# Optimization experiments

Measured on AMD Instinct MI355X. Metric: run time of the kernel, lower is better.

Reference implementation:

```python
import jax, jax.numpy as jnp
import numpy as np
from jax import lax

DIM = 128
N_CODEBOOKS = 8
CODEBOOK_SIZE = 2048
BATCH = 16
TOKENS = 2048


def setup_inputs() -> dict:
    key = jax.random.key(0)
    k1, k2 = jax.random.split(key)
    x = jax.random.normal(k1, (BATCH, DIM, TOKENS), dtype=jnp.float32)
    # matches nn.Parameter(torch.randn(K, D) / D**0.5) per stage, stacked
    codebooks = jax.random.normal(k2, (N_CODEBOOKS, CODEBOOK_SIZE, DIM),
                                  dtype=jnp.float32) / jnp.sqrt(jnp.float32(DIM))
    return {"x": x, "codebooks": codebooks}


def reference(x, codebooks):
    """Residual VQ forward.

    x: (B, D, T), codebooks: (n_cb, K, D)
    Returns (total_quantized (B,D,T), codes (B,n_cb,T) int32, commitment_loss scalar)
    """
    xt = jnp.transpose(x, (0, 2, 1))  # (B, T, D)

    def step(carry, cb):
        residual, total = carry  # (B,T,D) each; cb: (K,D)
        # squared euclidean distances: ||r||^2 - 2 r.c + ||c||^2 -> (B,T,K)
        dist = (jnp.sum(residual * residual, axis=-1, keepdims=True)
                - 2.0 * jnp.einsum('btd,kd->btk', residual, cb)
                + jnp.sum(cb * cb, axis=-1))
        idx = jnp.argmin(dist, axis=-1)          # (B, T)
        quantized = cb[idx]                       # gather -> (B, T, D)
        # straight-through combine
        q_st = residual + lax.stop_gradient(quantized - residual)
        total = total + q_st
        residual = residual - lax.stop_gradient(quantized)
        # F.mse_loss(residual.detach(), zeros) == mean(residual**2), detached
        loss = jnp.mean(lax.stop_gradient(residual) ** 2)
        return (residual, total), (idx.astype(jnp.int32), loss)

    init = (xt, jnp.zeros_like(xt))
    (_, total), (codes, losses) = lax.scan(step, init, codebooks)
    total_quantized = jnp.transpose(total, (0, 2, 1))   # (B, D, T)
    codes = jnp.transpose(codes, (1, 0, 2))             # (B, n_cb, T)
    commitment_loss = jnp.sum(losses)
    return total_quantized, codes, commitment_loss
```

## Files before the change

kernel.cpp:

```cpp
#include <hip/hip_runtime.h>

#define DIM 128
#define NCB 8
#define KSZ 2048
#define BATCH 16
#define TOK 2048
#define NTOK (BATCH * TOK)
#define NELEM (BATCH * DIM * TOK)
#define T_TILE 64
#define NTHR 512
#define CHUNK 64
#define HCHUNKS 16

typedef float f32x4 __attribute__((ext_vector_type(4)));
typedef short s16x8 __attribute__((ext_vector_type(8)));

__device__ __forceinline__ unsigned short f2bf(float f) {
    unsigned u = __float_as_uint(f);
    u = (u + 0x7FFFu + ((u >> 16) & 1u)) >> 16;
    return (unsigned short)u;
}
__device__ __forceinline__ float bf2f(unsigned short h) {
    return __uint_as_float(((unsigned)h) << 16);
}

__global__ void rvq_prep_hi(const float* __restrict__ cbs,
                            unsigned short* __restrict__ ch) {
    int i = blockIdx.x * 256 + threadIdx.x;
    ch[i] = f2bf(cbs[i]);
}

__global__ void rvq_cnorm(const float* __restrict__ cbs,
                          float* __restrict__ cnorm,
                          float* __restrict__ loss_acc) {
    if (blockIdx.x == 0 && threadIdx.x == 0) *loss_acc = 0.0f;
    int k = blockIdx.x * 256 + threadIdx.x;
    const float4* row = (const float4*)(cbs + (size_t)k * DIM);
    float s = 0.0f;
#pragma unroll
    for (int i = 0; i < DIM / 4; ++i) {
        float4 v = row[i];
        s += v.x * v.x + v.y * v.y + v.z * v.z + v.w * v.w;
    }
    cnorm[k] = s;
}

__global__ __launch_bounds__(NTHR, 4) void rvq_fused(
        const float* __restrict__ x,
        const float* __restrict__ cbs,
        const unsigned short* __restrict__ ch,
        const float* __restrict__ cng,
        float* __restrict__ out,
        float* __restrict__ codes,
        float* __restrict__ loss_acc) {
    __shared__ float res_lds[T_TILE][DIM + 2];
    __shared__ __align__(16) unsigned char uni[32768];
    unsigned short* Bb = (unsigned short*)uni;
    float*          mv1 = (float*)uni;
    float*          mv2 = (float*)(uni + 8192);
    unsigned short* mi1 = (unsigned short*)(uni + 16384);
    unsigned short* mi2 = (unsigned short*)(uni + 20480);
    unsigned short (*best4s)[4] = (unsigned short(*)[4])(uni + 24576);

    const int tid   = threadIdx.x;
    const int lane  = tid & 63;
    const int wv    = __builtin_amdgcn_readfirstlane(tid >> 6);
    const int col16 = lane & 15;
    const int quad  = lane >> 4;
    const int h2    = wv & 1;
    const int wg    = wv >> 1;

    const int token0 = blockIdx.x * T_TILE;
    const int b      = token0 >> 11;
    const int t_in_b = token0 & (TOK - 1);

    {
        const float* xb = x + (size_t)b * DIM * TOK + t_in_b;
#pragma unroll
        for (int it = 0; it < 4; ++it) {
            int idx = it * NTHR + tid;
            int d  = idx >> 4;
            int t4 = (idx & 15) * 4;
            float4 v = *(const float4*)(xb + (size_t)d * TOK + t4);
            res_lds[t4 + 0][d] = v.x;
            res_lds[t4 + 1][d] = v.y;
            res_lds[t4 + 2][d] = v.z;
            res_lds[t4 + 3][d] = v.w;
        }
    }
    __syncthreads();

    float my_loss = 0.0f;

#define STAGE_LOAD(cc)                                                         \
    {                                                                          \
        const unsigned short* _p = ch_s +                                      \
            ((size_t)(h2 * 1024 + (cc) * CHUNK + wg * 16 + col16)) * DIM +     \
            quad * 8;                                                          \
        stg0 = *(const s16x8*)(_p + 0);                                        \
        stg1 = *(const s16x8*)(_p + 32);                                       \
        stg2 = *(const s16x8*)(_p + 64);                                       \
        stg3 = *(const s16x8*)(_p + 96);                                       \
    }

#define STAGE_WRITE()                                                          \
    {                                                                          \
        unsigned short* _bh = Bb + h2 * 8192;                                  \
        *(s16x8*)&_bh[(wg * 4 + 0) * 512 + lane * 8] = stg0;                   \
        *(s16x8*)&_bh[(wg * 4 + 1) * 512 + lane * 8] = stg1;                   \
        *(s16x8*)&_bh[(wg * 4 + 2) * 512 + lane * 8] = stg2;                   \
        *(s16x8*)&_bh[(wg * 4 + 3) * 512 + lane * 8] = stg3;                   \
    }

#define COMPUTE_FOLD(cc)                                                       \
    {                                                                          \
        const unsigned short* _bh = Bb + h2 * 8192;                            \
        f32x4 a0 = (f32x4){0.f, 0.f, 0.f, 0.f};                                \
        f32x4 a1 = a0, a2 = a0, a3 = a0;                                       \
        _Pragma("unroll")                                                      \
        for (int dc = 0; dc < 4; ++dc) {                                       \
            s16x8 b0 = *(const s16x8*)&_bh[(0  + dc) * 512 + lane * 8];        \
            s16x8 b1 = *(const s16x8*)&_bh[(4  + dc) * 512 + lane * 8];        \
            s16x8 b2 = *(const s16x8*)&_bh[(8  + dc) * 512 + lane * 8];        \
            s16x8 b3 = *(const s16x8*)&_bh[(12 + dc) * 512 + lane * 8];        \
            a0 = __builtin_amdgcn_mfma_f32_16x16x32_bf16(ah[dc], b0, a0, 0, 0, 0); \
            a1 = __builtin_amdgcn_mfma_f32_16x16x32_bf16(ah[dc], b1, a1, 0, 0, 0); \
            a2 = __builtin_amdgcn_mfma_f32_16x16x32_bf16(ah[dc], b2, a2, 0, 0, 0); \
            a3 = __builtin_amdgcn_mfma_f32_16x16x32_bf16(ah[dc], b3, a3, 0, 0, 0); \
            a0 = __builtin_amdgcn_mfma_f32_16x16x32_bf16(al[dc], b0, a0, 0, 0, 0); \
            a1 = __builtin_amdgcn_mfma_f32_16x16x32_bf16(al[dc], b1, a1, 0, 0, 0); \
            a2 = __builtin_amdgcn_mfma_f32_16x16x32_bf16(al[dc], b2, a2, 0, 0, 0); \
            a3 = __builtin_amdgcn_mfma_f32_16x16x32_bf16(al[dc], b3, a3, 0, 0, 0); \
        }                                                                      \
        const int _ib0 = h2 * 1024 + (cc) * CHUNK + col16;                     \
        const float _cn0 = cn_s[_ib0], _cn1 = cn_s[_ib0 + 16];                 \
        const float _cn2 = cn_s[_ib0 + 32], _cn3 = cn_s[_ib0 + 48];            \
        _Pragma("unroll")                                                      \
        for (int r = 0; r < 4; ++r) {                                          \
            float p0 = fmaf(-2.0f, a0[r], _cn0);                               \
            float p1 = fmaf(-2.0f, a1[r], _cn1);                               \
            float p2 = fmaf(-2.0f, a2[r], _cn2);                               \
            float p3 = fmaf(-2.0f, a3[r], _cn3);                               \
            bool c01 = p1 < p0;                                                \
            float m01 = c01 ? p1 : p0; int j01 = c01 ? _ib0 + 16 : _ib0;       \
            bool c23 = p3 < p2;                                                \
            float m23 = c23 ? p3 : p2; int j23 = c23 ? _ib0 + 48 : _ib0 + 32;  \
            bool cf = m23 < m01;                                               \
            float m = cf ? m23 : m01; int jm = cf ? j23 : j01;                 \
            bool b1 = m < v1[r];                                               \
            bool b2 = m < v2[r];                                               \
            v2[r] = b1 ? v1[r] : (b2 ? m : v2[r]);                             \
            i2[r] = b1 ? i1[r] : (b2 ? jm : i2[r]);                            \
            v1[r] = b1 ? m : v1[r];                                            \
            i1[r] = b1 ? jm : i1[r];                                           \
        }                                                                      \
    }

#pragma unroll 1
    for (int s = 0; s < NCB; ++s) {
        const unsigned short* __restrict__ ch_s = ch  + (size_t)s * KSZ * DIM;
        const float* __restrict__ cb_s = cbs + (size_t)s * KSZ * DIM;
        const float* __restrict__ cn_s = cng + (size_t)s * KSZ;

        s16x8 stg0, stg1, stg2, stg3;

        STAGE_LOAD(0);

        s16x8 ah[4], al[4];
#pragma unroll
        for (int dc = 0; dc < 4; ++dc) {
            int t  = wg * 16 + col16;
            int d0 = dc * 32 + quad * 8;
            float4 u = *(const float4*)&res_lds[t][d0];
            float4 w = *(const float4*)&res_lds[t][d0 + 4];
            float e[8] = {u.x, u.y, u.z, u.w, w.x, w.y, w.z, w.w};
            s16x8 hv, lv;
#pragma unroll
            for (int j = 0; j < 8; ++j) {
                unsigned short hb = f2bf(e[j]);
                hv[j] = (short)hb;
                lv[j] = (short)f2bf(e[j] - bf2f(hb));
            }
            ah[dc] = hv; al[dc] = lv;
        }

        float v1[4], v2[4]; int i1[4], i2[4];
#pragma unroll
        for (int r = 0; r < 4; ++r) {
            v1[r] = 3.4e38f; v2[r] = 3.4e38f; i1[r] = 0; i2[r] = 0;
        }

        STAGE_WRITE(); __syncthreads();
#pragma unroll 1
        for (int cc = 0; cc < HCHUNKS - 1; ++cc) {
            STAGE_LOAD(cc + 1);
            COMPUTE_FOLD(cc);
            __syncthreads();
            STAGE_WRITE();
            __syncthreads();
        }
        COMPUTE_FOLD(HCHUNKS - 1);
        __syncthreads();

#pragma unroll
        for (int r = 0; r < 4; ++r) {
            int t = wg * 16 + quad * 4 + r;
            int o = t * 32 + h2 * 16 + col16;
            mv1[o] = v1[r];
            mi1[o] = (unsigned short)i1[r];
            mv2[o] = v2[r];
            mi2[o] = (unsigned short)i2[r];
        }
        __syncthreads();

        {
            const int mt = tid >> 3;
            const int c8 = tid & 7;
            float bv[4] = {3.4e38f, 3.4e38f, 3.4e38f, 3.4e38f};
            int   bi[4] = {0x7FFFFFFF, 0x7FFFFFFF, 0x7FFFFFFF, 0x7FFFFFFF};
            const float* MV = (c8 & 4) ? mv2 : mv1;
            const unsigned short* MI = (c8 & 4) ? mi2 : mi1;
            const int base = mt * 32 + (c8 & 3) * 8;
            const float4 va = *(const float4*)&MV[base];
            const float4 vb = *(const float4*)&MV[base + 4];
            const s16x8  qi = *(const s16x8*)&MI[base];
            float vv[8] = {va.x, va.y, va.z, va.w, vb.x, vb.y, vb.z, vb.w};
#pragma unroll
            for (int c = 0; c < 8; ++c) {
                float v = vv[c]; int i = (int)(unsigned short)qi[c];
#pragma unroll
                for (int j = 0; j < 4; ++j) {
                    if (v < bv[j] || (v == bv[j] && i < bi[j])) {
                        float tv = bv[j]; bv[j] = v; v = tv;
                        int   ti = bi[j]; bi[j] = i; i = ti;
                    }
                }
            }
#pragma unroll
            for (int mk = 1; mk <= 4; mk <<= 1) {
                float ov[4]; int oi[4];
#pragma unroll
                for (int j = 0; j < 4; ++j) {
                    ov[j] = __shfl_xor(bv[j], mk, 64);
                    oi[j] = __shfl_xor(bi[j], mk, 64);
                }
#pragma unroll
                for (int c = 0; c < 4; ++c) {
                    float v = ov[c]; int i = oi[c];
#pragma unroll
                    for (int j = 0; j < 4; ++j) {
                        if (v < bv[j] || (v == bv[j] && i < bi[j])) {
                            float tv = bv[j]; bv[j] = v; v = tv;
                            int   ti = bi[j]; bi[j] = i; i = ti;
                        }
                    }
                }
            }
            if (c8 < 4) best4s[mt][c8] = (unsigned short)bi[c8];
        }
        __syncthreads();

        {
            const int t  = tid >> 3;
            const int c8 = tid & 7;
            const int cand = best4s[t][c8 & 3];
            const float* crow = cb_s + (size_t)cand * DIM;
            float n0 = 0, n1 = 0, n2 = 0, n3 = 0;
            float a0 = 0, a1 = 0, a2 = 0, a3 = 0;
#pragma unroll 8
            for (int d4 = 0; d4 < DIM / 4; ++d4) {
                float4 r4 = *(const float4*)&res_lds[t][d4 * 4];
                float4 q4 = *(const float4*)&crow[d4 * 4];
                n0 = fmaf(r4.x, r4.x, n0); n1 = fmaf(r4.y, r4.y, n1);
                n2 = fmaf(r4.z, r4.z, n2); n3 = fmaf(r4.w, r4.w, n3);
                a0 = fmaf(r4.x, q4.x, a0); a1 = fmaf(r4.y, q4.y, a1);
                a2 = fmaf(r4.z, q4.z, a2); a3 = fmaf(r4.w, q4.w, a3);
            }
            float rn  = (n0 + n1) + (n2 + n3);
            float dot = (a0 + a1) + (a2 + a3);
            float dist = fmaf(-2.0f, dot, rn) + cn_s[cand];
            int best = cand;
#pragma unroll
            for (int mk = 1; mk <= 2; mk <<= 1) {
                float od = __shfl_xor(dist, mk, 64);
                int   oi = __shfl_xor(best, mk, 64);
                if (od < dist || (od == dist && oi < best)) {
                    dist = od; best = oi;
                }
            }
            if (c8 == 0)
                codes[(size_t)b * (NCB * TOK) + (size_t)s * TOK + t_in_b + t] =
                    (float)best;
            const float* qrow = cb_s + (size_t)best * DIM;
            float lp = 0.0f;
#pragma unroll
            for (int k4 = 0; k4 < 4; ++k4) {
                int d = c8 * 16 + k4 * 4;
                float4 r4 = *(const float4*)&res_lds[t][d];
                float4 q4 = *(const float4*)&qrow[d];
                float4 nr;
                nr.x = r4.x - q4.x; nr.y = r4.y - q4.y;
                nr.z = r4.z - q4.z; nr.w = r4.w - q4.w;
                *(float4*)&res_lds[t][d] = nr;
                lp += nr.x * nr.x + nr.y * nr.y + nr.z * nr.z + nr.w * nr.w;
            }
            my_loss += lp;
        }
        __syncthreads();
    }

    {
        const float* xb = x + (size_t)b * DIM * TOK + t_in_b;
        float* ob = out + (size_t)b * DIM * TOK + t_in_b;
#pragma unroll
        for (int it = 0; it < 4; ++it) {
            int idx = it * NTHR + tid;
            int d  = idx >> 4;
            int t4 = (idx & 15) * 4;
            float4 v = *(const float4*)(xb + (size_t)d * TOK + t4);
            float4 o;
            o.x = v.x - res_lds[t4 + 0][d];
            o.y = v.y - res_lds[t4 + 1][d];
            o.z = v.z - res_lds[t4 + 2][d];
            o.w = v.w - res_lds[t4 + 3][d];
            *(float4*)(ob + (size_t)d * TOK + t4) = o;
        }
    }

#pragma unroll
    for (int off = 32; off > 0; off >>= 1)
        my_loss += __shfl_down(my_loss, off, 64);
    if (lane == 0) atomicAdd(loss_acc, my_loss);
}

__global__ void rvq_loss_fin(const float* __restrict__ loss_acc,
                             float* __restrict__ loss_out) {
    *loss_out = *loss_acc * (1.0f / (float)NELEM);
}

extern "C" void kernel_launch(void* const* d_in, const int* in_sizes, int n_in,
                              void* d_out, int out_size, void* d_ws, size_t ws_size,
                              hipStream_t stream) {
    const float* x   = (const float*)d_in[0];
    const float* cbs = (const float*)d_in[1];

    float* out      = (float*)d_out;
    float* codes    = out + NELEM;
    float* loss_out = out + NELEM + (size_t)BATCH * NCB * TOK;

    float* wsf      = (float*)d_ws;
    float* loss_acc = wsf;
    unsigned short* ch = (unsigned short*)(wsf + 256);
    float* cng = (float*)(ch + (size_t)NCB * KSZ * DIM);

    hipLaunchKernelGGL(rvq_prep_hi, dim3((NCB * KSZ * DIM) / 256), dim3(256),
                       0, stream, cbs, ch);
    hipLaunchKernelGGL(rvq_cnorm, dim3((NCB * KSZ) / 256), dim3(256), 0, stream,
                       cbs, cng, loss_acc);
    hipLaunchKernelGGL(rvq_fused, dim3(NTOK / T_TILE), dim3(NTHR), 0, stream,
                       x, cbs, ch, cng, out, codes, loss_acc);
    hipLaunchKernelGGL(rvq_loss_fin, dim3(1), dim3(1), 0, stream,
                       loss_acc, loss_out);
}
```

Baseline: 574.4 us.

## Shrink token tile, keep residuals in registers, double-buffer codebook via LDS DMA

Each block now handles 32 tokens with 2 waves instead of 64 tokens with 8 waves. Each wave scans the full codebook for its 16 tokens, where before the codebook was split into halves across wave pairs. Residuals stay in registers across stages instead of shared memory, and codebook chunks are double-buffered into LDS with global_load_lds, which drops the register staging and one barrier per chunk. MFMA sections get raised wave priority. The cost is twice as many blocks, each reading the whole codebook per stage, so total codebook traffic per token tile doubles, and occupancy now depends on register pressure from the rr array.

```diff
diff --git a/kernel.cpp b/kernel.cpp
--- a/kernel.cpp
+++ b/kernel.cpp
@@ -7,10 +7,10 @@
 #define TOK 2048
 #define NTOK (BATCH * TOK)
 #define NELEM (BATCH * DIM * TOK)
-#define T_TILE 64
-#define NTHR 512
+#define T_TILE 32
+#define NTHR 128
 #define CHUNK 64
-#define HCHUNKS 16
+#define NCHUNK (KSZ / CHUNK)
 
 typedef float f32x4 __attribute__((ext_vector_type(4)));
 typedef short s16x8 __attribute__((ext_vector_type(8)));
@@ -22,6 +22,12 @@
 }
 __device__ __forceinline__ float bf2f(unsigned short h) {
     return __uint_as_float(((unsigned)h) << 16);
+}
+
+__device__ __forceinline__ void gll16(const void* g, void* l) {
+    __builtin_amdgcn_global_load_lds(
+        (const __attribute__((address_space(1))) unsigned int*)g,
+        (__attribute__((address_space(3))) unsigned int*)l, 16, 0, 0);
 }
 
 __global__ void rvq_prep_hi(const float* __restrict__ cbs,
@@ -45,7 +51,7 @@
     cnorm[k] = s;
 }
 
-__global__ __launch_bounds__(NTHR, 4) void rvq_fused(
+__global__ __launch_bounds__(NTHR, 2) void rvq_fused(
         const float* __restrict__ x,
         const float* __restrict__ cbs,
         const unsigned short* __restrict__ ch,
@@ -53,22 +59,22 @@
         float* __restrict__ out,
         float* __restrict__ codes,
         float* __restrict__ loss_acc) {
-    __shared__ float res_lds[T_TILE][DIM + 2];
-    __shared__ __align__(16) unsigned char uni[32768];
-    unsigned short* Bb = (unsigned short*)uni;
+    __shared__ __attribute__((aligned(16))) unsigned char uni[32768];
+    __shared__ unsigned short best4s[T_TILE][4];
+
+    unsigned short* Bb  = (unsigned short*)uni;
+    float*          xs  = (float*)uni;
     float*          mv1 = (float*)uni;
-    float*          mv2 = (float*)(uni + 8192);
-    unsigned short* mi1 = (unsigned short*)(uni + 16384);
-    unsigned short* mi2 = (unsigned short*)(uni + 20480);
-    unsigned short (*best4s)[4] = (unsigned short(*)[4])(uni + 24576);
+    float*          mv2 = (float*)(uni + 2048);
+    unsigned short* mi1 = (unsigned short*)(uni + 4096);
+    unsigned short* mi2 = (unsigned short*)(uni + 5120);
 
     const int tid   = threadIdx.x;
     const int lane  = tid & 63;
     const int wv    = __builtin_amdgcn_readfirstlane(tid >> 6);
     const int col16 = lane & 15;
     const int quad  = lane >> 4;
-    const int h2    = wv & 1;
-    const int wg    = wv >> 1;
+    const int t_loc = wv * 16 + col16;
 
     const int token0 = blockIdx.x * T_TILE;
     const int b      = token0 >> 11;
@@ -77,46 +83,49 @@
     {
         const float* xb = x + (size_t)b * DIM * TOK + t_in_b;
 #pragma unroll
-        for (int it = 0; it < 4; ++it) {
+        for (int it = 0; it < 8; ++it) {
             int idx = it * NTHR + tid;
-            int d  = idx >> 4;
-            int t4 = (idx & 15) * 4;
+            int d  = idx >> 3;
+            int t4 = (idx & 7) * 4;
             float4 v = *(const float4*)(xb + (size_t)d * TOK + t4);
-            res_lds[t4 + 0][d] = v.x;
-            res_lds[t4 + 1][d] = v.y;
-            res_lds[t4 + 2][d] = v.z;
-            res_lds[t4 + 3][d] = v.w;
+            xs[(t4 + 0) * DIM + d] = v.x;
+            xs[(t4 + 1) * DIM + d] = v.y;
+            xs[(t4 + 2) * DIM + d] = v.z;
+            xs[(t4 + 3) * DIM + d] = v.w;
         }
     }
     __syncthreads();
 
+    float rr[4][8];
+#pragma unroll
+    for (int dc = 0; dc < 4; ++dc) {
+        float4 u = *(const float4*)&xs[t_loc * DIM + dc * 32 + quad * 8];
+        float4 w = *(const float4*)&xs[t_loc * DIM + dc * 32 + quad * 8 + 4];
+        rr[dc][0] = u.x; rr[dc][1] = u.y; rr[dc][2] = u.z; rr[dc][3] = u.w;
+        rr[dc][4] = w.x; rr[dc][5] = w.y; rr[dc][6] = w.z; rr[dc][7] = w.w;
+    }
+    __syncthreads();
+
     float my_loss = 0.0f;
 
-#define STAGE_LOAD(cc)                                                         \
+#define STAGE_GLL(bsel, cc)                                                    \
     {                                                                          \
-        const unsigned short* _p = ch_s +                                      \
-            ((size_t)(h2 * 1024 + (cc) * CHUNK + wg * 16 + col16)) * DIM +     \
-            quad * 8;                                                          \
-        stg0 = *(const s16x8*)(_p + 0);                                        \
-        stg1 = *(const s16x8*)(_p + 32);                                       \
-        stg2 = *(const s16x8*)(_p + 64);                                       \
-        stg3 = *(const s16x8*)(_p + 96);                                       \
-    }
-
-#define STAGE_WRITE()                                                          \
+        _Pragma("unroll")                                                      \
+        for (int i = 0; i < 8; ++i) {                                          \
+            int f = wv * 8 + i;                                                \
+            const unsigned short* gp = ch_s +                                  \
+                ((size_t)((cc) * CHUNK + (f >> 2) * 16 + col16)) * DIM +       \
+                ((f & 3) * 32 + quad * 8);                                     \
+            gll16(gp, Bb + (bsel) * 8192 + f * 512);                           \
+        }                                                                      \
+    }
+
+#define COMPUTE_FOLD(cc, bsel)                                                 \
     {                                                                          \
-        unsigned short* _bh = Bb + h2 * 8192;                                  \
-        *(s16x8*)&_bh[(wg * 4 + 0) * 512 + lane * 8] = stg0;                   \
-        *(s16x8*)&_bh[(wg * 4 + 1) * 512 + lane * 8] = stg1;                   \
-        *(s16x8*)&_bh[(wg * 4 + 2) * 512 + lane * 8] = stg2;                   \
-        *(s16x8*)&_bh[(wg * 4 + 3) * 512 + lane * 8] = stg3;                   \
-    }
-
-#define COMPUTE_FOLD(cc)                                                       \
-    {                                                                          \
-        const unsigned short* _bh = Bb + h2 * 8192;                            \
+        const unsigned short* _bh = Bb + (bsel) * 8192;                        \
         f32x4 a0 = (f32x4){0.f, 0.f, 0.f, 0.f};                                \
         f32x4 a1 = a0, a2 = a0, a3 = a0;                                       \
+        __builtin_amdgcn_s_setprio(1);                                         \
         _Pragma("unroll")                                                      \
         for (int dc = 0; dc < 4; ++dc) {                                       \
             s16x8 b0 = *(const s16x8*)&_bh[(0  + dc) * 512 + lane * 8];        \
@@ -132,7 +141,8 @@
             a2 = __builtin_amdgcn_mfma_f32_16x16x32_bf16(al[dc], b2, a2, 0, 0, 0); \
             a3 = __builtin_amdgcn_mfma_f32_16x16x32_bf16(al[dc], b3, a3, 0, 0, 0); \
         }                                                                      \
-        const int _ib0 = h2 * 1024 + (cc) * CHUNK + col16;                     \
+        __builtin_amdgcn_s_setprio(0);                                         \
+        const int _ib0 = (cc) * CHUNK + col16;                                 \
         const float _cn0 = cn_s[_ib0], _cn1 = cn_s[_ib0 + 16];                 \
         const float _cn2 = cn_s[_ib0 + 32], _cn3 = cn_s[_ib0 + 48];            \
         _Pragma("unroll")                                                      \
@@ -162,24 +172,17 @@
         const float* __restrict__ cb_s = cbs + (size_t)s * KSZ * DIM;
         const float* __restrict__ cn_s = cng + (size_t)s * KSZ;
 
-        s16x8 stg0, stg1, stg2, stg3;
-
-        STAGE_LOAD(0);
+        STAGE_GLL(0, 0);
 
         s16x8 ah[4], al[4];
 #pragma unroll
         for (int dc = 0; dc < 4; ++dc) {
-            int t  = wg * 16 + col16;
-            int d0 = dc * 32 + quad * 8;
-            float4 u = *(const float4*)&res_lds[t][d0];
-            float4 w = *(const float4*)&res_lds[t][d0 + 4];
-            float e[8] = {u.x, u.y, u.z, u.w, w.x, w.y, w.z, w.w};
             s16x8 hv, lv;
 #pragma unroll
             for (int j = 0; j < 8; ++j) {
-                unsigned short hb = f2bf(e[j]);
+                unsigned short hb = f2bf(rr[dc][j]);
                 hv[j] = (short)hb;
-                lv[j] = (short)f2bf(e[j] - bf2f(hb));
+                lv[j] = (short)f2bf(rr[dc][j] - bf2f(hb));
             }
             ah[dc] = hv; al[dc] = lv;
         }
@@ -190,22 +193,21 @@
             v1[r] = 3.4e38f; v2[r] = 3.4e38f; i1[r] = 0; i2[r] = 0;
         }
 
-        STAGE_WRITE(); __syncthreads();
+        __syncthreads();
+
 #pragma unroll 1
-        for (int cc = 0; cc < HCHUNKS - 1; ++cc) {
-            STAGE_LOAD(cc + 1);
-            COMPUTE_FOLD(cc);
+        for (int cc = 0; cc < NCHUNK - 1; ++cc) {
+            STAGE_GLL((cc + 1) & 1, cc + 1);
+            COMPUTE_FOLD(cc, cc & 1);
             __syncthreads();
-            STAGE_WRITE();
-            __syncthreads();
-        }
-        COMPUTE_FOLD(HCHUNKS - 1);
+        }
+        COMPUTE_FOLD(NCHUNK - 1, 1);
         __syncthreads();
 
 #pragma unroll
         for (int r = 0; r < 4; ++r) {
-            int t = wg * 16 + quad * 4 + r;
-            int o = t * 32 + h2 * 16 + col16;
+            int t = wv * 16 + quad * 4 + r;
+            int o = t * 16 + col16;
             mv1[o] = v1[r];
             mi1[o] = (unsigned short)i1[r];
             mv2[o] = v2[r];
@@ -214,20 +216,21 @@
         __syncthreads();
 
         {
-            const int mt = tid >> 3;
-            const int c8 = tid & 7;
+            const int mt = tid >> 2;
+            const int cs = tid & 3;
             float bv[4] = {3.4e38f, 3.4e38f, 3.4e38f, 3.4e38f};
             int   bi[4] = {0x7FFFFFFF, 0x7FFFFFFF, 0x7FFFFFFF, 0x7FFFFFFF};
-            const float* MV = (c8 & 4) ? mv2 : mv1;
-            const unsigned short* MI = (c8 & 4) ? mi2 : mi1;
-            const int base = mt * 32 + (c8 & 3) * 8;
-            const float4 va = *(const float4*)&MV[base];
-            const float4 vb = *(const float4*)&MV[base + 4];
-            const s16x8  qi = *(const s16x8*)&MI[base];
-            float vv[8] = {va.x, va.y, va.z, va.w, vb.x, vb.y, vb.z, vb.w};
+            const float4  cv1 = *(const float4*)&mv1[tid * 4];
+            const float4  cv2 = *(const float4*)&mv2[tid * 4];
+            const ushort4 ci1 = *(const ushort4*)&mi1[tid * 4];
+            const ushort4 ci2 = *(const ushort4*)&mi2[tid * 4];
+            float vv[8] = {cv1.x, cv1.y, cv1.z, cv1.w,
+                           cv2.x, cv2.y, cv2.z, cv2.w};
+            int   ii[8] = {ci1.x, ci1.y, ci1.z, ci1.w,
+                           ci2.x, ci2.y, ci2.z, ci2.w};
 #pragma unroll
             for (int c = 0; c < 8; ++c) {
-                float v = vv[c]; int i = (int)(unsigned short)qi[c];
+                float v = vv[c]; int i = ii[c];
 #pragma unroll
                 for (int j = 0; j < 4; ++j) {
                     if (v < bv[j] || (v == bv[j] && i < bi[j])) {
@@ -237,7 +240,7 @@
                 }
             }
 #pragma unroll
-            for (int mk = 1; mk <= 4; mk <<= 1) {
+            for (int mk = 1; mk <= 2; mk <<= 1) {
                 float ov[4]; int oi[4];
 #pragma unroll
                 for (int j = 0; j < 4; ++j) {
@@ -256,73 +259,108 @@
                     }
                 }
             }
-            if (c8 < 4) best4s[mt][c8] = (unsigned short)bi[c8];
+            best4s[mt][cs] = (unsigned short)bi[cs];
         }
         __syncthreads();
 
         {
-            const int t  = tid >> 3;
-            const int c8 = tid & 7;
-            const int cand = best4s[t][c8 & 3];
-            const float* crow = cb_s + (size_t)cand * DIM;
-            float n0 = 0, n1 = 0, n2 = 0, n3 = 0;
-            float a0 = 0, a1 = 0, a2 = 0, a3 = 0;
-#pragma unroll 8
-            for (int d4 = 0; d4 < DIM / 4; ++d4) {
-                float4 r4 = *(const float4*)&res_lds[t][d4 * 4];
-                float4 q4 = *(const float4*)&crow[d4 * 4];
-                n0 = fmaf(r4.x, r4.x, n0); n1 = fmaf(r4.y, r4.y, n1);
-                n2 = fmaf(r4.z, r4.z, n2); n3 = fmaf(r4.w, r4.w, n3);
-                a0 = fmaf(r4.x, q4.x, a0); a1 = fmaf(r4.y, q4.y, a1);
-                a2 = fmaf(r4.z, q4.z, a2); a3 = fmaf(r4.w, q4.w, a3);
+            const int c0 = best4s[t_loc][0];
+            const int c1 = best4s[t_loc][1];
+            const int c2 = best4s[t_loc][2];
+            const int c3 = best4s[t_loc][3];
+            float rnp = 0.f;
+#pragma unroll
+            for (int dc = 0; dc < 4; ++dc)
+#pragma unroll
+                for (int j = 0; j < 8; ++j)
+                    rnp = fmaf(rr[dc][j], rr[dc][j], rnp);
+            float dp0 = 0.f, dp1 = 0.f, dp2 = 0.f, dp3 = 0.f;
+#pragma unroll
+            for (int dc = 0; dc < 4; ++dc) {
+                const int doff = dc * 32 + quad * 8;
+                const float4 qa0 = *(const float4*)(cb_s + (size_t)c0 * DIM + doff);
+                const float4 qb0 = *(const float4*)(cb_s + (size_t)c0 * DIM + doff + 4);
+                const float4 qa1 = *(const float4*)(cb_s + (size_t)c1 * DIM + doff);
+                const float4 qb1 = *(const float4*)(cb_s + (size_t)c1 * DIM + doff + 4);
+                const float4 qa2 = *(const float4*)(cb_s + (size_t)c2 * DIM + doff);
+                const float4 qb2 = *(const float4*)(cb_s + (size_t)c2 * DIM + doff + 4);
+                const float4 qa3 = *(const float4*)(cb_s + (size_t)c3 * DIM + doff);
+                const float4 qb3 = *(const float4*)(cb_s + (size_t)c3 * DIM + doff + 4);
+                dp0 = fmaf(rr[dc][0], qa0.x, dp0); dp0 = fmaf(rr[dc][1], qa0.y, dp0);
+                dp0 = fmaf(rr[dc][2], qa0.z, dp0); dp0 = fmaf(rr[dc][3], qa0.w, dp0);
+                dp0 = fmaf(rr[dc][4], qb0.x, dp0); dp0 = fmaf(rr[dc][5], qb0.y, dp0);
+                dp0 = fmaf(rr[dc][6], qb0.z, dp0); dp0 = fmaf(rr[dc][7], qb0.w, dp0);
+                dp1 = fmaf(rr[dc][0], qa1.x, dp1); dp1 = fmaf(rr[dc][1], qa1.y, dp1);
+                dp1 = fmaf(rr[dc][2], qa1.z, dp1); dp1 = fmaf(rr[dc][3], qa1.w, dp1);
+                dp1 = fmaf(rr[dc][4], qb1.x, dp1); dp1 = fmaf(rr[dc][5], qb1.y, dp1);
+                dp1 = fmaf(rr[dc][6], qb1.z, dp1); dp1 = fmaf(rr[dc][7], qb1.w, dp1);
+                dp2 = fmaf(rr[dc][0], qa2.x, dp2); dp2 = fmaf(rr[dc][1], qa2.y, dp2);
+                dp2 = fmaf(rr[dc][2], qa2.z, dp2); dp2 = fmaf(rr[dc][3], qa2.w, dp2);
+                dp2 = fmaf(rr[dc][4], qb2.x, dp2); dp2 = fmaf(rr[dc][5], qb2.y, dp2);
+                dp2 = fmaf(rr[dc][6], qb2.z, dp2); dp2 = fmaf(rr[dc][7], qb2.w, dp2);
+                dp3 = fmaf(rr[dc][0], qa3.x, dp3); dp3 = fmaf(rr[dc][1], qa3.y, dp3);
+                dp3 = fmaf(rr[dc][2], qa3.z, dp3); dp3 = fmaf(rr[dc][3], qa3.w, dp3);
+                dp3 = fmaf(rr[dc][4], qb3.x, dp3); dp3 = fmaf(rr[dc][5], qb3.y, dp3);
+                dp3 = fmaf(rr[dc][6], qb3.z, dp3); dp3 = fmaf(rr[dc][7], qb3.w, dp3);
             }
-            float rn  = (n0 + n1) + (n2 + n3);
-            float dot = (a0 + a1) + (a2 + a3);
-            float dist = fmaf(-2.0f, dot, rn) + cn_s[cand];
-            int best = cand;
-#pragma unroll
-            for (int mk = 1; mk <= 2; mk <<= 1) {
-                float od = __shfl_xor(dist, mk, 64);
-                int   oi = __shfl_xor(best, mk, 64);
-                if (od < dist || (od == dist && oi < best)) {
-                    dist = od; best = oi;
+            rnp += __shfl_xor(rnp, 16, 64); rnp += __shfl_xor(rnp, 32, 64);
+            dp0 += __shfl_xor(dp0, 16, 64); dp0 += __shfl_xor(dp0, 32, 64);
+            dp1 += __shfl_xor(dp1, 16, 64); dp1 += __shfl_xor(dp1, 32, 64);
+            dp2 += __shfl_xor(dp2, 16, 64); dp2 += __shfl_xor(dp2, 32, 64);
+            dp3 += __shfl_xor(dp3, 16, 64); dp3 += __shfl_xor(dp3, 32, 64);
+            float d0 = fmaf(-2.0f, dp0, rnp) + cn_s[c0];
+            float d1 = fmaf(-2.0f, dp1, rnp) + cn_s[c1];
+            float d2 = fmaf(-2.0f, dp2, rnp) + cn_s[c2];
+            float d3 = fmaf(-2.0f, dp3, rnp) + cn_s[c3];
+            float bd = d0; int bw = c0;
+            if (d1 < bd || (d1 == bd && c1 < bw)) { bd = d1; bw = c1; }
+            if (d2 < bd || (d2 == bd && c2 < bw)) { bd = d2; bw = c2; }
+            if (d3 < bd || (d3 == bd && c3 < bw)) { bd = d3; bw = c3; }
+            if (quad == 0)
+                codes[(size_t)b * (NCB * TOK) + (size_t)s * TOK + t_in_b + t_loc] =
+                    (float)bw;
+            float lp = 0.0f;
+#pragma unroll
+            for (int dc = 0; dc < 4; ++dc) {
+                const float4 qa =
+                    *(const float4*)(cb_s + (size_t)bw * DIM + dc * 32 + quad * 8);
+                const float4 qb =
+                    *(const float4*)(cb_s + (size_t)bw * DIM + dc * 32 + quad * 8 + 4);
+                float q[8] = {qa.x, qa.y, qa.z, qa.w, qb.x, qb.y, qb.z, qb.w};
+#pragma unroll
+                for (int j = 0; j < 8; ++j) {
+                    float rf = rr[dc][j] - q[j];
+                    rr[dc][j] = rf;
+                    lp = fmaf(rf, rf, lp);
                 }
             }
-            if (c8 == 0)
-                codes[(size_t)b * (NCB * TOK) + (size_t)s * TOK + t_in_b + t] =
-                    (float)best;
-            const float* qrow = cb_s + (size_t)best * DIM;
-            float lp = 0.0f;
-#pragma unroll
-            for (int k4 = 0; k4 < 4; ++k4) {
-                int d = c8 * 16 + k4 * 4;
-                float4 r4 = *(const float4*)&res_lds[t][d];
-                float4 q4 = *(const float4*)&qrow[d];
-                float4 nr;
-                nr.x = r4.x - q4.x; nr.y = r4.y - q4.y;
-                nr.z = r4.z - q4.z; nr.w = r4.w - q4.w;
-                *(float4*)&res_lds[t][d] = nr;
-                lp += nr.x * nr.x + nr.y * nr.y + nr.z * nr.z + nr.w * nr.w;
-            }
             my_loss += lp;
         }
-        __syncthreads();
-    }
-
+    }
+
+    __syncthreads();
+#pragma unroll
+    for (int dc = 0; dc < 4; ++dc) {
+        *(float4*)&xs[t_loc * DIM + dc * 32 + quad * 8] =
+            (float4){rr[dc][0], rr[dc][1], rr[dc][2], rr[dc][3]};
+        *(float4*)&xs[t_loc * DIM + dc * 32 + quad * 8 + 4] =
+            (float4){rr[dc][4], rr[dc][5], rr[dc][6], rr[dc][7]};
+    }
+    __syncthreads();
     {
         const float* xb = x + (size_t)b * DIM * TOK + t_in_b;
         float* ob = out + (size_t)b * DIM * TOK + t_in_b;
 #pragma unroll
-        for (int it = 0; it < 4; ++it) {
+        for (int it = 0; it < 8; ++it) {
             int idx = it * NTHR + tid;
-            int d  = idx >> 4;
-            int t4 = (idx & 15) * 4;
+            int d  = idx >> 3;
+            int t4 = (idx & 7) * 4;
             float4 v = *(const float4*)(xb + (size_t)d * TOK + t4);
             float4 o;
-            o.x = v.x - res_lds[t4 + 0][d];
-            o.y = v.y - res_lds[t4 + 1][d];
-            o.z = v.z - res_lds[t4 + 2][d];
-            o.w = v.w - res_lds[t4 + 3][d];
+            o.x = v.x - xs[(t4 + 0) * DIM + d];
+            o.y = v.y - xs[(t4 + 1) * DIM + d];
+            o.z = v.z - xs[(t4 + 2) * DIM + d];
+            o.w = v.w - xs[(t4 + 3) * DIM + d];
             *(float4*)(ob + (size_t)d * TOK + t4) = o;
         }
     }
```

Result: slower. 760.7 us (+32.4%).
